# Optimization experiments

Hardware: AMD Instinct MI355X
Metric: run time of the kernel (lower is better)

Reference implementation:

```python
import jax, jax.numpy as jnp
import numpy as np

NUM_HEADS = 16
EPS = 1e-5


def _layernorm(x, w):
    # torch LayerNorm (biased variance), bias=False
    m = jnp.mean(x, axis=-1, keepdims=True)
    v = jnp.mean(jnp.square(x - m), axis=-1, keepdims=True)
    return (x - m) * jax.lax.rsqrt(v + EPS) * w


def setup_inputs() -> dict:
    key = jax.random.key(0)
    ks = jax.random.split(key, 8)
    B, S, H, A = 2, 2048, 1024, 1024
    hd = H // NUM_HEADS
    return {
        "x": jax.random.normal(ks[0], (B, S, H), jnp.float32),
        "ada_cond": jax.random.normal(ks[1], (B, A), jnp.float32),
        "freqs": jax.random.normal(ks[2], (S, hd // 2, 2), jnp.float32),
        "w_qkv": jax.random.normal(ks[3], (3 * H, H), jnp.float32) * (1.0 / np.sqrt(H)),
        "w_o": jax.random.normal(ks[4], (H, H), jnp.float32) * (1.0 / np.sqrt(H)),
        "ln_w": jnp.ones((H,), jnp.float32),
        "mod_w": jax.random.normal(ks[5], (3 * H, A), jnp.float32) * 0.02,
        "mod_b": jax.random.normal(ks[6], (3 * H,), jnp.float32) * 0.02,
        "qn_w": jnp.ones((hd,), jnp.float32),
        "kn_w": jnp.ones((hd,), jnp.float32),
    }


def reference(x, ada_cond, freqs, w_qkv, w_o, ln_w, mod_w, mod_b, qn_w, kn_w):
    B, S, H = x.shape
    nh = NUM_HEADS
    hd = H // nh

    # pre-norm + AdaLN modulation (with gate)
    h = _layernorm(x, ln_w)
    mod = (jax.nn.silu(ada_cond) @ mod_w.T + mod_b)[:, None, :]  # [B,1,3H]
    scale, shift, gate = jnp.split(mod, 3, axis=-1)
    h = h * (scale + 1.0) + shift

    # QKV projection and head split
    qkv = h @ w_qkv.T                                  # [B,S,3H]
    q, k, v = jnp.split(qkv, 3, axis=-1)
    to_heads = lambda t: t.reshape(B, S, nh, hd).transpose(0, 2, 1, 3)  # [B,nh,S,hd]
    q, k, v = to_heads(q), to_heads(k), to_heads(v)

    # per-head QK layernorm
    q = _layernorm(q, qn_w)
    k = _layernorm(k, kn_w)

    # RoPE (complex rotation via interleaved pairs)
    f = freqs[:S].reshape(1, 1, S, hd // 2, 2)

    def rope(t):
        tr = t.reshape(B, nh, S, hd // 2, 2)
        re = tr[..., 0] * f[..., 0] - tr[..., 1] * f[..., 1]
        im = tr[..., 1] * f[..., 0] + tr[..., 0] * f[..., 1]
        return jnp.stack([re, im], axis=-1).reshape(B, nh, S, hd)

    q, k = rope(q), rope(k)

    # scaled dot-product attention (non-causal)
    scores = jnp.einsum("bhqd,bhkd->bhqk", q, k) * (1.0 / np.sqrt(hd))
    attn = jax.nn.softmax(scores, axis=-1)
    o = jnp.einsum("bhqk,bhkd->bhqd", attn, v)
    o = o.transpose(0, 2, 1, 3).reshape(B, S, H)

    return (o @ w_o.T) * gate
```

## Files before the change

### kernel.cpp

```cpp
#include <hip/hip_runtime.h>
#include <hip/hip_bf16.h>
#include <math.h>

#define B_ 2
#define S_ 2048
#define H_ 1024
#define A_ 1024
#define NH_ 16
#define HD_ 64
#define H3_ 3072
#define EPS_ 1e-5f

typedef __attribute__((ext_vector_type(8))) short short8;
typedef __attribute__((ext_vector_type(4))) float floatx4;

__device__ inline unsigned short f2bf(float x) {
    union { float f; unsigned u; } v; v.f = x;
    unsigned r = v.u + 0x7fffu + ((v.u >> 16) & 1u);
    return (unsigned short)(r >> 16);
}

__device__ inline unsigned pk_bf16(float a, float b) {
    union { __hip_bfloat162 h; unsigned u; } v;
    v.h = __float22bfloat162_rn(make_float2(a, b));
    return v.u;
}

__device__ inline void gld_lds16(const void* g, void* l) {
    __builtin_amdgcn_global_load_lds(
        (const __attribute__((address_space(1))) unsigned int*)g,
        (__attribute__((address_space(3))) unsigned int*)l, 16, 0, 0);
}

#define TBLK(r) ((((r) >> 3) * 544) + (((r) & 7) * 64))

__global__ __launch_bounds__(256) void cast_bf16_kernel(
    const float* __restrict__ in, unsigned short* __restrict__ out, int n)
{
    int i = (blockIdx.x * 256 + threadIdx.x) * 8;
    if (i >= n) return;
    float4 a = *(const float4*)(in + i);
    float4 b = *(const float4*)(in + i + 4);
    uint4 o;
    o.x = pk_bf16(a.x, a.y);
    o.y = pk_bf16(a.z, a.w);
    o.z = pk_bf16(b.x, b.y);
    o.w = pk_bf16(b.z, b.w);
    *(uint4*)(out + i) = o;
}

__global__ __launch_bounds__(256) void mod_gemv_kernel(
    const float* __restrict__ ada, const float* __restrict__ mod_w,
    const float* __restrict__ mod_b, float* __restrict__ mod)
{
    int wid = threadIdx.x >> 6;
    int lane = threadIdx.x & 63;
    int idx = blockIdx.x * 4 + wid;
    int b = idx / H3_;
    int j = idx % H3_;
    const float* ar = ada + (size_t)b * A_;
    const float* wr = mod_w + (size_t)j * A_;
    float acc = 0.f;
    for (int a = lane; a < A_; a += 64) {
        float av = ar[a];
        float sv = av / (1.f + __expf(-av));
        acc += sv * wr[a];
    }
    #pragma unroll
    for (int m = 1; m < 64; m <<= 1) acc += __shfl_xor(acc, m);
    if (lane == 0) mod[idx] = acc + mod_b[j];
}

__global__ __launch_bounds__(256) void ln_mod_kernel(
    const float* __restrict__ x, const float* __restrict__ ln_w,
    const float* __restrict__ mod, unsigned short* __restrict__ hout)
{
    int row = blockIdx.x;
    int b = row >> 11;
    const float* xr = x + (size_t)row * H_;
    int t = threadIdx.x;
    float4 xv = *(const float4*)(xr + t * 4);
    float s1 = xv.x + xv.y + xv.z + xv.w;
    float s2 = xv.x*xv.x + xv.y*xv.y + xv.z*xv.z + xv.w*xv.w;
    #pragma unroll
    for (int m = 1; m < 64; m <<= 1) { s1 += __shfl_xor(s1, m); s2 += __shfl_xor(s2, m); }
    __shared__ float r1[4], r2[4];
    int wid = t >> 6, lane = t & 63;
    if (lane == 0) { r1[wid] = s1; r2[wid] = s2; }
    __syncthreads();
    s1 = r1[0] + r1[1] + r1[2] + r1[3];
    s2 = r2[0] + r2[1] + r2[2] + r2[3];
    float mean = s1 * (1.f / H_);
    float var  = s2 * (1.f / H_) - mean * mean;
    float rstd = rsqrtf(var + EPS_);
    const float* mrow = mod + (size_t)b * H3_;
    float4 wv = *(const float4*)(ln_w + t * 4);
    float4 sc = *(const float4*)(mrow + t * 4);
    float4 sh = *(const float4*)(mrow + H_ + t * 4);
    float4 hv;
    hv.x = (xv.x - mean) * rstd * wv.x * (sc.x + 1.f) + sh.x;
    hv.y = (xv.y - mean) * rstd * wv.y * (sc.y + 1.f) + sh.y;
    hv.z = (xv.z - mean) * rstd * wv.z * (sc.z + 1.f) + sh.z;
    hv.w = (xv.w - mean) * rstd * wv.w * (sc.w + 1.f) + sh.w;
    uint2 o;
    o.x = pk_bf16(hv.x, hv.y);
    o.y = pk_bf16(hv.z, hv.w);
    *(uint2*)(hout + (size_t)row * H_ + t * 4) = o;
}

__global__ __launch_bounds__(256) void gemm_qkv_fused_kernel(
    const unsigned short* __restrict__ A, const unsigned short* __restrict__ Bm,
    const float* __restrict__ freqs, const float* __restrict__ qn_w,
    const float* __restrict__ kn_w, unsigned short* __restrict__ qout,
    unsigned short* __restrict__ kout, unsigned short* __restrict__ vtout)
{
    __shared__ unsigned short As[128 * 32];
    __shared__ unsigned short Bs[128 * 32];
    const int K = H_, N = H3_;
    int t = threadIdx.x;
    int w = t >> 6, lane = t & 63;
    int q16 = lane & 15, quad = lane >> 4;
    int wm = w >> 1, wn = w & 1;
    int m0 = blockIdx.y * 128, n0 = blockIdx.x * 128;

    int srow = (w << 5) + (lane >> 2);
    int soff = (lane & 3) << 3;
    const unsigned short* ga = A + (size_t)(m0 + srow) * K + soff;
    const unsigned short* gb = Bm + (size_t)(n0 + srow) * K + soff;
    unsigned short* la0 = As + (w << 5) * 32;
    unsigned short* la1 = la0 + 16 * 32;
    unsigned short* lb0 = Bs + (w << 5) * 32;
    unsigned short* lb1 = lb0 + 16 * 32;

    floatx4 acc[4][4];
    #pragma unroll
    for (int mt = 0; mt < 4; ++mt)
        #pragma unroll
        for (int nt = 0; nt < 4; ++nt)
            acc[mt][nt] = (floatx4){0.f, 0.f, 0.f, 0.f};

    int a_row = wm * 64 + q16;
    int b_row = wn * 64 + q16;

    for (int kt = 0; kt < K; kt += 32) {
        __syncthreads();
        gld_lds16(ga, la0);
        gld_lds16(ga + (size_t)16 * K, la1);
        gld_lds16(gb, lb0);
        gld_lds16(gb + (size_t)16 * K, lb1);
        ga += 32; gb += 32;
        __syncthreads();

        short8 af[4], bf[4];
        #pragma unroll
        for (int mt = 0; mt < 4; ++mt)
            af[mt] = *(const short8*)&As[(a_row + mt * 16) * 32 + quad * 8];
        #pragma unroll
        for (int nt = 0; nt < 4; ++nt)
            bf[nt] = *(const short8*)&Bs[(b_row + nt * 16) * 32 + quad * 8];
        #pragma unroll
        for (int mt = 0; mt < 4; ++mt)
            #pragma unroll
            for (int nt = 0; nt < 4; ++nt)
                acc[mt][nt] = __builtin_amdgcn_mfma_f32_16x16x32_bf16(
                    af[mt], bf[nt], acc[mt][nt], 0, 0, 0);
    }

    int n_base = n0 + wn * 64;
    int sec = n_base >> 10;
    int head = (n_base & 1023) >> 6;

    if (sec == 2) {
        #pragma unroll
        for (int mt = 0; mt < 4; ++mt) {
            int m = m0 + wm * 64 + mt * 16 + quad * 4;
            int b = m >> 11, s = m & (S_ - 1);
            #pragma unroll
            for (int nt = 0; nt < 4; ++nt) {
                int d = nt * 16 + q16;
                unsigned short* dst =
                    vtout + ((size_t)((b * 16 + head) * 64 + d)) * S_ + s;
                uint2 pk;
                pk.x = pk_bf16(acc[mt][nt][0], acc[mt][nt][1]);
                pk.y = pk_bf16(acc[mt][nt][2], acc[mt][nt][3]);
                *(uint2*)dst = pk;
            }
        }
    } else {
        const float* nw = (sec == 0) ? qn_w : kn_w;
        float w4[4];
        #pragma unroll
        for (int nt = 0; nt < 4; ++nt) w4[nt] = nw[nt * 16 + q16];
        unsigned short* outp = (sec == 0) ? qout : kout;
        float qscale = (sec == 0) ? 0.1803368801111244f : 1.0f;

        #pragma unroll
        for (int mt = 0; mt < 4; ++mt) {
            #pragma unroll
            for (int i = 0; i < 4; ++i) {
                int m = m0 + wm * 64 + mt * 16 + quad * 4 + i;
                int b = m >> 11, s = m & (S_ - 1);
                float v0 = acc[mt][0][i], v1 = acc[mt][1][i];
                float v2 = acc[mt][2][i], v3 = acc[mt][3][i];
                float s1 = (v0 + v1) + (v2 + v3);
                float s2 = (v0 * v0 + v1 * v1) + (v2 * v2 + v3 * v3);
                #pragma unroll
                for (int msk = 1; msk < 16; msk <<= 1) {
                    s1 += __shfl_xor(s1, msk);
                    s2 += __shfl_xor(s2, msk);
                }
                float mean = s1 * (1.f / 64);
                float var  = s2 * (1.f / 64) - mean * mean;
                float rstd = rsqrtf(var + EPS_);
                float vv[4];
                vv[0] = (v0 - mean) * rstd * w4[0];
                vv[1] = (v1 - mean) * rstd * w4[1];
                vv[2] = (v2 - mean) * rstd * w4[2];
                vv[3] = (v3 - mean) * rstd * w4[3];
                const float* fr = freqs + (size_t)s * 64;
                unsigned short* orow = outp + ((size_t)((b * 16 + head) * S_ + s)) * 64;
                #pragma unroll
                for (int nt = 0; nt < 4; ++nt) {
                    int c = nt * 16 + q16;
                    float vp = __shfl_xor(vv[nt], 1);
                    float2 ff = *(const float2*)(fr + (c & ~1));
                    float r = (c & 1) ? (vv[nt] * ff.x + vp * ff.y)
                                      : (vv[nt] * ff.x - vp * ff.y);
                    orow[c] = f2bf(r * qscale);
                }
            }
        }
    }
}

__global__ __launch_bounds__(256) void gemm_bt_bf16_kernel(
    const unsigned short* __restrict__ A, const unsigned short* __restrict__ Bm,
    float* __restrict__ C, int M, int N, int K,
    const float* __restrict__ gate, int gate_stride, int batch_shift)
{
    __shared__ unsigned short As[128 * 32];
    __shared__ unsigned short Bs[128 * 32];
    int t = threadIdx.x;
    int w = t >> 6, lane = t & 63;
    int q16 = lane & 15, quad = lane >> 4;
    int wm = w >> 1, wn = w & 1;
    int m0 = blockIdx.y * 128, n0 = blockIdx.x * 128;

    int srow = (w << 5) + (lane >> 2);
    int soff = (lane & 3) << 3;
    const unsigned short* ga = A + (size_t)(m0 + srow) * K + soff;
    const unsigned short* gb = Bm + (size_t)(n0 + srow) * K + soff;
    unsigned short* la0 = As + (w << 5) * 32;
    unsigned short* la1 = la0 + 16 * 32;
    unsigned short* lb0 = Bs + (w << 5) * 32;
    unsigned short* lb1 = lb0 + 16 * 32;

    floatx4 acc[4][4];
    #pragma unroll
    for (int mt = 0; mt < 4; ++mt)
        #pragma unroll
        for (int nt = 0; nt < 4; ++nt)
            acc[mt][nt] = (floatx4){0.f, 0.f, 0.f, 0.f};

    int a_row = wm * 64 + q16;
    int b_row = wn * 64 + q16;

    for (int kt = 0; kt < K; kt += 32) {
        __syncthreads();
        gld_lds16(ga, la0);
        gld_lds16(ga + (size_t)16 * K, la1);
        gld_lds16(gb, lb0);
        gld_lds16(gb + (size_t)16 * K, lb1);
        ga += 32; gb += 32;
        __syncthreads();

        short8 af[4], bf[4];
        #pragma unroll
        for (int mt = 0; mt < 4; ++mt)
            af[mt] = *(const short8*)&As[(a_row + mt * 16) * 32 + quad * 8];
        #pragma unroll
        for (int nt = 0; nt < 4; ++nt)
            bf[nt] = *(const short8*)&Bs[(b_row + nt * 16) * 32 + quad * 8];
        #pragma unroll
        for (int mt = 0; mt < 4; ++mt)
            #pragma unroll
            for (int nt = 0; nt < 4; ++nt)
                acc[mt][nt] = __builtin_amdgcn_mfma_f32_16x16x32_bf16(
                    af[mt], bf[nt], acc[mt][nt], 0, 0, 0);
    }

    #pragma unroll
    for (int mt = 0; mt < 4; ++mt) {
        #pragma unroll
        for (int i = 0; i < 4; ++i) {
            int m = m0 + wm * 64 + mt * 16 + quad * 4 + i;
            float* crow = C + (size_t)m * N;
            const float* grow = gate ? gate + (size_t)(m >> batch_shift) * gate_stride
                                     : nullptr;
            #pragma unroll
            for (int nt = 0; nt < 4; ++nt) {
                int n = n0 + wn * 64 + nt * 16 + q16;
                float v = acc[mt][nt][i];
                if (gate) v *= grow[n];
                crow[n] = v;
            }
        }
    }
}

__global__ __launch_bounds__(256) void attn_mfma_kernel(
    const unsigned short* __restrict__ q, const unsigned short* __restrict__ k,
    const unsigned short* __restrict__ vt, unsigned short* __restrict__ o)
{
    __shared__ unsigned short Ks[8 * 544];
    __shared__ unsigned short Vs[8 * 544];
    __shared__ unsigned short Ps[4][16][72];

    int t = threadIdx.x;
    int w = t >> 6, lane = t & 63;
    int q16 = lane & 15, quad = lane >> 4;
    int bh = blockIdx.y, b = bh >> 4, h = bh & 15;
    int s0 = blockIdx.x * 64;

    const unsigned short* qg = q + ((size_t)bh * S_ + s0) * HD_;
    gld_lds16(qg + (2 * w) * 512 + lane * 8, &Ks[(2 * w) * 544]);
    gld_lds16(qg + (2 * w + 1) * 512 + lane * 8, &Ks[(2 * w + 1) * 544]);
    __syncthreads();
    int qrow = TBLK(16 * w + q16);
    short8 qf0 = *(const short8*)&Ks[qrow + quad * 8];
    short8 qf1 = *(const short8*)&Ks[qrow + 32 + quad * 8];

    short8 ones8;
    #pragma unroll
    for (int i = 0; i < 8; ++i) ones8[i] = (short)0x3F80;

    floatx4 acc_o[4];
    floatx4 acc_l = (floatx4){0.f, 0.f, 0.f, 0.f};
    #pragma unroll
    for (int i = 0; i < 4; ++i) acc_o[i] = (floatx4){0.f, 0.f, 0.f, 0.f};

    const unsigned short* kg = k + (size_t)bh * S_ * HD_;
    const unsigned short* vg = vt + (size_t)bh * 64 * S_;
    int vsrc = (16 * w + (lane >> 3)) * S_ + (lane & 7) * 8;

    for (int kt = 0; kt < S_ / 64; ++kt) {
        __syncthreads();
        gld_lds16(kg + (2 * w) * 512 + lane * 8, &Ks[(2 * w) * 544]);
        gld_lds16(kg + (2 * w + 1) * 512 + lane * 8, &Ks[(2 * w + 1) * 544]);
        gld_lds16(vg + vsrc, &Vs[(2 * w) * 544]);
        gld_lds16(vg + vsrc + 8 * S_, &Vs[(2 * w + 1) * 544]);
        kg += 64 * HD_;
        vg += 64;
        __syncthreads();

        floatx4 sc[4];
        #pragma unroll
        for (int nk = 0; nk < 4; ++nk) sc[nk] = (floatx4){-12.f, -12.f, -12.f, -12.f};
        #pragma unroll
        for (int nk = 0; nk < 4; ++nk) {
            int krow = TBLK(16 * nk + q16);
            short8 kf0 = *(const short8*)&Ks[krow + quad * 8];
            short8 kf1 = *(const short8*)&Ks[krow + 32 + quad * 8];
            sc[nk] = __builtin_amdgcn_mfma_f32_16x16x32_bf16(kf0, qf0, sc[nk], 0, 0, 0);
            sc[nk] = __builtin_amdgcn_mfma_f32_16x16x32_bf16(kf1, qf1, sc[nk], 0, 0, 0);
        }

        #pragma unroll
        for (int nk = 0; nk < 4; ++nk) {
            float p0 = __builtin_amdgcn_exp2f(sc[nk][0]);
            float p1 = __builtin_amdgcn_exp2f(sc[nk][1]);
            float p2 = __builtin_amdgcn_exp2f(sc[nk][2]);
            float p3 = __builtin_amdgcn_exp2f(sc[nk][3]);
            uint2 pk;
            pk.x = pk_bf16(p0, p1);
            pk.y = pk_bf16(p2, p3);
            *(uint2*)&Ps[w][q16][16 * nk + quad * 4] = pk;
        }

        __asm__ __volatile__("" ::: "memory");

        #pragma unroll
        for (int ks = 0; ks < 2; ++ks) {
            short8 pf = *(const short8*)&Ps[w][q16][ks * 32 + quad * 8];
            acc_l = __builtin_amdgcn_mfma_f32_16x16x32_bf16(ones8, pf, acc_l, 0, 0, 0);
            #pragma unroll
            for (int nd = 0; nd < 4; ++nd) {
                short8 vf = *(const short8*)&Vs[TBLK(16 * nd + q16) + ks * 32 + quad * 8];
                acc_o[nd] = __builtin_amdgcn_mfma_f32_16x16x32_bf16(vf, pf, acc_o[nd], 0, 0, 0);
            }
        }
    }

    float inv = 1.f / acc_l[0];
    #pragma unroll
    for (int nd = 0; nd < 4; ++nd) {
        uint2 pk;
        pk.x = pk_bf16(acc_o[nd][0] * inv, acc_o[nd][1] * inv);
        pk.y = pk_bf16(acc_o[nd][2] * inv, acc_o[nd][3] * inv);
        *(uint2*)&Ps[w][q16][16 * nd + quad * 4] = pk;
    }
    __asm__ __volatile__("" ::: "memory");
    unsigned short* og = o + ((size_t)(b * S_ + s0 + 16 * w + q16)) * H_ + h * HD_;
    #pragma unroll
    for (int i = 0; i < 2; ++i) {
        int c = quad * 2 + i;
        *(short8*)(og + c * 8) = *(const short8*)&Ps[w][q16][c * 8];
    }
}

extern "C" void kernel_launch(void* const* d_in, const int* in_sizes, int n_in,
                              void* d_out, int out_size, void* d_ws, size_t ws_size,
                              hipStream_t stream)
{
    const float* x     = (const float*)d_in[0];
    const float* ada   = (const float*)d_in[1];
    const float* freqs = (const float*)d_in[2];
    const float* w_qkv = (const float*)d_in[3];
    const float* w_o   = (const float*)d_in[4];
    const float* ln_w  = (const float*)d_in[5];
    const float* mod_w = (const float*)d_in[6];
    const float* mod_b = (const float*)d_in[7];
    const float* qn_w  = (const float*)d_in[8];
    const float* kn_w  = (const float*)d_in[9];
    float* out = (float*)d_out;

    float* ws  = (float*)d_ws;
    float* mod = ws;
    unsigned short* hb    = (unsigned short*)(mod + 8192);
    unsigned short* qb    = hb + (size_t)B_ * S_ * H_;
    unsigned short* kb    = qb + (size_t)B_ * S_ * H_;
    unsigned short* vtb   = kb + (size_t)B_ * S_ * H_;
    unsigned short* ob    = vtb + (size_t)B_ * S_ * H_;
    unsigned short* wqkvb = ob + (size_t)B_ * S_ * H_;
    unsigned short* wob   = wqkvb + (size_t)H3_ * H_;

    cast_bf16_kernel<<<H3_ * H_ / (8 * 256), 256, 0, stream>>>(w_qkv, wqkvb, H3_ * H_);
    cast_bf16_kernel<<<H_ * H_ / (8 * 256), 256, 0, stream>>>(w_o, wob, H_ * H_);
    mod_gemv_kernel<<<B_ * H3_ / 4, 256, 0, stream>>>(ada, mod_w, mod_b, mod);
    ln_mod_kernel<<<B_ * S_, 256, 0, stream>>>(x, ln_w, mod, hb);
    gemm_qkv_fused_kernel<<<dim3(H3_ / 128, B_ * S_ / 128), 256, 0, stream>>>(
        hb, wqkvb, freqs, qn_w, kn_w, qb, kb, vtb);
    attn_mfma_kernel<<<dim3(S_ / 64, B_ * NH_), 256, 0, stream>>>(qb, kb, vtb, ob);
    gemm_bt_bf16_kernel<<<dim3(H_ / 128, B_ * S_ / 128), 256, 0, stream>>>(
        ob, wob, out, B_ * S_, H_, H_, mod + 2 * H_, H3_, 11);
}
```

Baseline: 262.7 us.

## Restructure attention to split keys across waves with register-resident P and fp16 V

The attention kernel now gives each wave a 16-key slice of every 64-key tile while all waves cover all 64 queries. Q fragments and K fragments live in registers, and K/V for the next tile are prefetched into registers. V is produced in fp16 so the 16x16x16 f16 MFMA can consume P directly from registers, which removes the P round-trip through LDS. Partial outputs and row sums from the four waves are reduced through shared memory at the end. In exchange this uses many more accumulator registers, adds a cross-wave reduction, and accepts fp16 range and rounding for V and P.

```diff
diff --git a/kernel.cpp b/kernel.cpp
--- a/kernel.cpp
+++ b/kernel.cpp
@@ -1,5 +1,6 @@
 #include <hip/hip_runtime.h>
 #include <hip/hip_bf16.h>
+#include <hip/hip_fp16.h>
 #include <math.h>
 
 #define B_ 2
@@ -13,6 +14,8 @@
 
 typedef __attribute__((ext_vector_type(8))) short short8;
 typedef __attribute__((ext_vector_type(4))) float floatx4;
+typedef __attribute__((ext_vector_type(4))) _Float16 half4v;
+typedef __attribute__((ext_vector_type(2))) __fp16 fp16x2;
 
 __device__ inline unsigned short f2bf(float x) {
     union { float f; unsigned u; } v; v.f = x;
@@ -26,13 +29,17 @@
     return v.u;
 }
 
+__device__ inline unsigned pk_f16(float a, float b) {
+    union { __half2 h; unsigned u; } v;
+    v.h = __float22half2_rn(make_float2(a, b));
+    return v.u;
+}
+
 __device__ inline void gld_lds16(const void* g, void* l) {
     __builtin_amdgcn_global_load_lds(
         (const __attribute__((address_space(1))) unsigned int*)g,
         (__attribute__((address_space(3))) unsigned int*)l, 16, 0, 0);
 }
-
-#define TBLK(r) ((((r) >> 3) * 544) + (((r) & 7) * 64))
 
 __global__ __launch_bounds__(256) void cast_bf16_kernel(
     const float* __restrict__ in, unsigned short* __restrict__ out, int n)
@@ -181,8 +188,8 @@
                 unsigned short* dst =
                     vtout + ((size_t)((b * 16 + head) * 64 + d)) * S_ + s;
                 uint2 pk;
-                pk.x = pk_bf16(acc[mt][nt][0], acc[mt][nt][1]);
-                pk.y = pk_bf16(acc[mt][nt][2], acc[mt][nt][3]);
+                pk.x = pk_f16(acc[mt][nt][0], acc[mt][nt][1]);
+                pk.y = pk_f16(acc[mt][nt][2], acc[mt][nt][3]);
                 *(uint2*)dst = pk;
             }
         }
@@ -308,13 +315,13 @@
     }
 }
 
-__global__ __launch_bounds__(256) void attn_mfma_kernel(
+__global__ __launch_bounds__(256, 2) void attn_mfma_kernel(
     const unsigned short* __restrict__ q, const unsigned short* __restrict__ k,
     const unsigned short* __restrict__ vt, unsigned short* __restrict__ o)
 {
-    __shared__ unsigned short Ks[8 * 544];
-    __shared__ unsigned short Vs[8 * 544];
-    __shared__ unsigned short Ps[4][16][72];
+    __shared__ __align__(16) unsigned char smem[16 * 1024];
+    __shared__ float lbuf[4][4][16];
+    unsigned short* Vs = (unsigned short*)smem;
 
     int t = threadIdx.x;
     int w = t >> 6, lane = t & 63;
@@ -322,89 +329,116 @@
     int bh = blockIdx.y, b = bh >> 4, h = bh & 15;
     int s0 = blockIdx.x * 64;
 
-    const unsigned short* qg = q + ((size_t)bh * S_ + s0) * HD_;
-    gld_lds16(qg + (2 * w) * 512 + lane * 8, &Ks[(2 * w) * 544]);
-    gld_lds16(qg + (2 * w + 1) * 512 + lane * 8, &Ks[(2 * w + 1) * 544]);
+    const unsigned short* qgp = q + ((size_t)bh * S_ + s0) * HD_;
+    short8 qf[4][2];
+    #pragma unroll
+    for (int qg = 0; qg < 4; ++qg)
+        #pragma unroll
+        for (int hh = 0; hh < 2; ++hh)
+            qf[qg][hh] = *(const short8*)(qgp + (16 * qg + q16) * HD_ + hh * 32 + quad * 8);
+
+    const unsigned short* kg = k + (size_t)bh * S_ * HD_ + (16 * w + q16) * HD_ + quad * 8;
+
+    const unsigned short* vg0 = vt + (size_t)bh * 64 * S_
+                              + (size_t)(16 * w + (lane >> 3)) * S_ + (lane & 7) * 8;
+    const unsigned short* vg1 = vg0 + 8 * S_;
+    unsigned short* vw0 = Vs + (16 * w + (lane >> 3)) * 64 + (((lane & 7) ^ (lane >> 3)) << 3);
+    unsigned short* vw1 = vw0 + 512;
+    int vroff = q16 * 64 + (((2 * w + (quad >> 1)) ^ (q16 & 7)) << 3) + ((quad & 1) << 2);
+
+    short8 kf_nx0 = *(const short8*)kg;
+    short8 kf_nx1 = *(const short8*)(kg + 32);
+    uint4 vr0 = *(const uint4*)vg0;
+    uint4 vr1 = *(const uint4*)vg1;
+
+    union { half4v h; uint2 u; } ones;
+    ones.u.x = 0x3C003C00u; ones.u.y = 0x3C003C00u;
+
+    floatx4 acc_o[4][4];
+    floatx4 acc_l[4];
+    #pragma unroll
+    for (int nd = 0; nd < 4; ++nd)
+        #pragma unroll
+        for (int qg = 0; qg < 4; ++qg)
+            acc_o[nd][qg] = (floatx4){0.f, 0.f, 0.f, 0.f};
+    #pragma unroll
+    for (int qg = 0; qg < 4; ++qg) acc_l[qg] = (floatx4){0.f, 0.f, 0.f, 0.f};
+
+    for (int kt = 0; kt < S_ / 64; ++kt) {
+        short8 kf0 = kf_nx0, kf1 = kf_nx1;
+        uint4 v0 = vr0, v1 = vr1;
+        __syncthreads();
+        *(uint4*)vw0 = v0;
+        *(uint4*)vw1 = v1;
+        __syncthreads();
+
+        if (kt + 1 < S_ / 64) {
+            kg += 64 * HD_; vg0 += 64; vg1 += 64;
+            kf_nx0 = *(const short8*)kg;
+            kf_nx1 = *(const short8*)(kg + 32);
+            vr0 = *(const uint4*)vg0;
+            vr1 = *(const uint4*)vg1;
+        }
+
+        floatx4 sc[4];
+        #pragma unroll
+        for (int qg = 0; qg < 4; ++qg) sc[qg] = (floatx4){-12.f, -12.f, -12.f, -12.f};
+        #pragma unroll
+        for (int qg = 0; qg < 4; ++qg) {
+            sc[qg] = __builtin_amdgcn_mfma_f32_16x16x32_bf16(kf0, qf[qg][0], sc[qg], 0, 0, 0);
+            sc[qg] = __builtin_amdgcn_mfma_f32_16x16x32_bf16(kf1, qf[qg][1], sc[qg], 0, 0, 0);
+        }
+
+        half4v vf[4];
+        #pragma unroll
+        for (int nd = 0; nd < 4; ++nd)
+            vf[nd] = *(const half4v*)&Vs[vroff + nd * 1024];
+
+        #pragma unroll
+        for (int qg = 0; qg < 4; ++qg) {
+            float p0 = __builtin_amdgcn_exp2f(sc[qg][0]);
+            float p1 = __builtin_amdgcn_exp2f(sc[qg][1]);
+            float p2 = __builtin_amdgcn_exp2f(sc[qg][2]);
+            float p3 = __builtin_amdgcn_exp2f(sc[qg][3]);
+            union { half4v h; fp16x2 f2[2]; } pf;
+            pf.f2[0] = __builtin_amdgcn_cvt_pkrtz(p0, p1);
+            pf.f2[1] = __builtin_amdgcn_cvt_pkrtz(p2, p3);
+            acc_l[qg] = __builtin_amdgcn_mfma_f32_16x16x16f16(ones.h, pf.h, acc_l[qg], 0, 0, 0);
+            #pragma unroll
+            for (int nd = 0; nd < 4; ++nd)
+                acc_o[nd][qg] = __builtin_amdgcn_mfma_f32_16x16x16f16(
+                    vf[nd], pf.h, acc_o[nd][qg], 0, 0, 0);
+        }
+    }
+
+    if (quad == 0) {
+        #pragma unroll
+        for (int qg = 0; qg < 4; ++qg) lbuf[w][qg][q16] = acc_l[qg][0];
+    }
     __syncthreads();
-    int qrow = TBLK(16 * w + q16);
-    short8 qf0 = *(const short8*)&Ks[qrow + quad * 8];
-    short8 qf1 = *(const short8*)&Ks[qrow + 32 + quad * 8];
-
-    short8 ones8;
-    #pragma unroll
-    for (int i = 0; i < 8; ++i) ones8[i] = (short)0x3F80;
-
-    floatx4 acc_o[4];
-    floatx4 acc_l = (floatx4){0.f, 0.f, 0.f, 0.f};
-    #pragma unroll
-    for (int i = 0; i < 4; ++i) acc_o[i] = (floatx4){0.f, 0.f, 0.f, 0.f};
-
-    const unsigned short* kg = k + (size_t)bh * S_ * HD_;
-    const unsigned short* vg = vt + (size_t)bh * 64 * S_;
-    int vsrc = (16 * w + (lane >> 3)) * S_ + (lane & 7) * 8;
-
-    for (int kt = 0; kt < S_ / 64; ++kt) {
-        __syncthreads();
-        gld_lds16(kg + (2 * w) * 512 + lane * 8, &Ks[(2 * w) * 544]);
-        gld_lds16(kg + (2 * w + 1) * 512 + lane * 8, &Ks[(2 * w + 1) * 544]);
-        gld_lds16(vg + vsrc, &Vs[(2 * w) * 544]);
-        gld_lds16(vg + vsrc + 8 * S_, &Vs[(2 * w + 1) * 544]);
-        kg += 64 * HD_;
-        vg += 64;
-        __syncthreads();
-
-        floatx4 sc[4];
-        #pragma unroll
-        for (int nk = 0; nk < 4; ++nk) sc[nk] = (floatx4){-12.f, -12.f, -12.f, -12.f};
-        #pragma unroll
-        for (int nk = 0; nk < 4; ++nk) {
-            int krow = TBLK(16 * nk + q16);
-            short8 kf0 = *(const short8*)&Ks[krow + quad * 8];
-            short8 kf1 = *(const short8*)&Ks[krow + 32 + quad * 8];
-            sc[nk] = __builtin_amdgcn_mfma_f32_16x16x32_bf16(kf0, qf0, sc[nk], 0, 0, 0);
-            sc[nk] = __builtin_amdgcn_mfma_f32_16x16x32_bf16(kf1, qf1, sc[nk], 0, 0, 0);
-        }
-
-        #pragma unroll
-        for (int nk = 0; nk < 4; ++nk) {
-            float p0 = __builtin_amdgcn_exp2f(sc[nk][0]);
-            float p1 = __builtin_amdgcn_exp2f(sc[nk][1]);
-            float p2 = __builtin_amdgcn_exp2f(sc[nk][2]);
-            float p3 = __builtin_amdgcn_exp2f(sc[nk][3]);
-            uint2 pk;
-            pk.x = pk_bf16(p0, p1);
-            pk.y = pk_bf16(p2, p3);
-            *(uint2*)&Ps[w][q16][16 * nk + quad * 4] = pk;
-        }
-
-        __asm__ __volatile__("" ::: "memory");
-
-        #pragma unroll
-        for (int ks = 0; ks < 2; ++ks) {
-            short8 pf = *(const short8*)&Ps[w][q16][ks * 32 + quad * 8];
-            acc_l = __builtin_amdgcn_mfma_f32_16x16x32_bf16(ones8, pf, acc_l, 0, 0, 0);
-            #pragma unroll
-            for (int nd = 0; nd < 4; ++nd) {
-                short8 vf = *(const short8*)&Vs[TBLK(16 * nd + q16) + ks * 32 + quad * 8];
-                acc_o[nd] = __builtin_amdgcn_mfma_f32_16x16x32_bf16(vf, pf, acc_o[nd], 0, 0, 0);
-            }
-        }
-    }
-
-    float inv = 1.f / acc_l[0];
+    float linv = 1.f / (lbuf[0][w][q16] + lbuf[1][w][q16] + lbuf[2][w][q16] + lbuf[3][w][q16]);
+
+    float* obuf = (float*)smem;
+    float* myw = obuf + ((w * 4) * 64 + lane) * 4;
+    float* myr = obuf + (w * 64 + lane) * 4;
+    unsigned short* og = o + ((size_t)(b * S_ + s0 + 16 * w + q16)) * H_ + h * HD_ + 4 * quad;
+
     #pragma unroll
     for (int nd = 0; nd < 4; ++nd) {
+        __syncthreads();
+        #pragma unroll
+        for (int qg = 0; qg < 4; ++qg)
+            *(floatx4*)(myw + qg * 256) = acc_o[nd][qg];
+        __syncthreads();
+        floatx4 r0 = *(const floatx4*)(myr);
+        floatx4 r1 = *(const floatx4*)(myr + 1024);
+        floatx4 r2 = *(const floatx4*)(myr + 2048);
+        floatx4 r3 = *(const floatx4*)(myr + 3072);
+        floatx4 s = (r0 + r1) + (r2 + r3);
         uint2 pk;
-        pk.x = pk_bf16(acc_o[nd][0] * inv, acc_o[nd][1] * inv);
-        pk.y = pk_bf16(acc_o[nd][2] * inv, acc_o[nd][3] * inv);
-        *(uint2*)&Ps[w][q16][16 * nd + quad * 4] = pk;
-    }
-    __asm__ __volatile__("" ::: "memory");
-    unsigned short* og = o + ((size_t)(b * S_ + s0 + 16 * w + q16)) * H_ + h * HD_;
-    #pragma unroll
-    for (int i = 0; i < 2; ++i) {
-        int c = quad * 2 + i;
-        *(short8*)(og + c * 8) = *(const short8*)&Ps[w][q16][c * 8];
+        pk.x = pk_bf16(s[0] * linv, s[1] * linv);
+        pk.y = pk_bf16(s[2] * linv, s[3] * linv);
+        *(uint2*)(og + nd * 16) = pk;
     }
 }
 
```

Result: no change. 263.1 us (+0.2%).
